# Kernel optimization log

Measured on AMD Instinct MI355X. Metric: run time of the kernel, lower is better.

## Reference

```python
import jax, jax.numpy as jnp
import numpy as np

N, E, G = 16384, 65536, 512
T, FIN, FOUT = 4, 128, 32
_DEG_HIST = np.array([1.0, 2.0, 3.0, 4.0])
AVG_LOG = float((np.log(np.arange(4) + 1.0) * _DEG_HIST).sum() / _DEG_HIST.sum())


def _bn(x, g, b, eps=1e-5):
    # BatchNorm1d in training mode: biased batch stats
    m = x.mean(0)
    v = x.var(0)
    return (x - m) * jax.lax.rsqrt(v + eps) * g + b


def _pna_conv(x, edge_index, ea_raw, We_c, be_c, Wpre, bpre, Wpost, bpost, Wlin, blin):
    src, dst = edge_index[0], edge_index[1]
    ea = ea_raw @ We_c + be_c                                   # conv-internal edge encoder [E,FIN]
    xt = jnp.broadcast_to(x[:, None, :], (N, T, FIN))           # towers share input (divide_input=False)
    h = jnp.concatenate([xt[dst], xt[src],
                         jnp.broadcast_to(ea[:, None, :], (E, T, FIN))], axis=-1)  # [E,T,3*FIN]
    m = jnp.einsum('etf,tfg->etg', h, Wpre) + bpre              # per-tower pre-NN [E,T,FIN]
    deg = jnp.clip(jax.ops.segment_sum(jnp.ones((E,), x.dtype), dst, N), 1.0)
    inv = (1.0 / deg)[:, None, None]
    mean = jax.ops.segment_sum(m, dst, N) * inv
    mean2 = jax.ops.segment_sum(m * m, dst, N) * inv
    std = jnp.sqrt(jax.nn.relu(mean2 - mean * mean) + 1e-5)
    mn = jax.ops.segment_min(m, dst, N)
    mx = jax.ops.segment_max(m, dst, N)
    mn = jnp.where(jnp.isfinite(mn), mn, 0.0)
    mx = jnp.where(jnp.isfinite(mx), mx, 0.0)
    agg = jnp.concatenate([mean, mn, mx, std], axis=-1)         # [N,T,4*FIN]
    s = (jnp.log(deg + 1.0) / AVG_LOG)[:, None, None]           # amplification scaler
    out = jnp.concatenate([agg, agg * s, agg / s], axis=-1)     # identity|amp|attenuation [N,T,12*FIN]
    out = jnp.concatenate([xt, out], axis=-1)                   # [N,T,13*FIN]
    out = jnp.einsum('ntf,tfg->ntg', out, Wpost) + bpost        # per-tower post-NN [N,T,FOUT]
    return out.reshape(N, T * FOUT) @ Wlin + blin               # tower mixing [N,FIN]


def setup_inputs() -> dict:
    key = jax.random.key(0)
    ks = jax.random.split(key, 24)
    def rn(k, shape, scale=0.05):
        return jax.random.normal(k, shape, dtype=jnp.float32) * scale
    return dict(
        x=jax.random.normal(ks[0], (N, 11), jnp.float32),
        edge_attr=jax.random.uniform(ks[1], (E, 4), jnp.float32),
        edge_index=jax.random.randint(ks[2], (2, E), 0, N),
        batch=jnp.sort(jax.random.randint(ks[3], (N,), 0, G)),
        Wa=rn(ks[4], (11, FIN), 0.2), ba=rn(ks[5], (FIN,)),
        We=rn(ks[6], (4, FIN), 0.2), be=rn(ks[7], (FIN,)),
        We_conv=rn(ks[8], (3, FIN, FIN)), be_conv=rn(ks[9], (3, FIN)),
        Wpre=rn(ks[10], (3, T, 3 * FIN, FIN)), bpre=rn(ks[11], (3, T, FIN)),
        Wpost=rn(ks[12], (3, T, 13 * FIN, FOUT)), bpost=rn(ks[13], (3, T, FOUT)),
        Wlin=rn(ks[14], (3, FIN, FIN)), blin=rn(ks[15], (3, FIN)),
        bng=1.0 + rn(ks[16], (3, FIN)), bnb=rn(ks[17], (3, FIN)),
        W1=rn(ks[18], (FIN, 64), 0.1), b1=rn(ks[19], (64,)),
        hg=1.0 + rn(ks[20], (64,)), hb=rn(ks[21], (64,)),
        W2=rn(ks[22], (64, 1), 0.1), b2=rn(ks[23], (1,)),
    )


def reference(x, edge_attr, edge_index, batch, Wa, ba, We, be,
              We_conv, be_conv, Wpre, bpre, Wpost, bpost, Wlin, blin,
              bng, bnb, W1, b1, hg, hb, W2, b2):
    h = jax.nn.relu(x @ Wa + ba)
    ea = jax.nn.relu(edge_attr @ We + be)
    for l in range(3):
        h = jax.nn.relu(_bn(_pna_conv(h, edge_index, ea, We_conv[l], be_conv[l],
                                      Wpre[l], bpre[l], Wpost[l], bpost[l],
                                      Wlin[l], blin[l]), bng[l], bnb[l]))
    cnt = jnp.clip(jax.ops.segment_sum(jnp.ones((N,), h.dtype), batch, G), 1.0)
    pooled = jax.ops.segment_sum(h, batch, G) / cnt[:, None]    # global_mean_pool
    z = jax.nn.relu(pooled @ W1 + b1)
    z = _bn(z, hg, hb)
    return (z @ W2 + b2).reshape(-1)
```

## Files before the change

### kernel.cpp

```cpp
#include <hip/hip_runtime.h>
#include <hip/hip_bf16.h>

#define DEVFN static __device__ __forceinline__

constexpr int NN = 16384;
constexpr int EE = 65536;
constexpr int GG = 512;
constexpr float AVG_LOG_F = 1.0227308671603782f;

typedef _Float16 hfrag __attribute__((ext_vector_type(8)));
typedef __attribute__((ext_vector_type(4))) float f4;

DEVFN unsigned short f2h(float f) {
  _Float16 h = (_Float16)f;
  unsigned short r; __builtin_memcpy(&r, &h, 2); return r;
}
DEVFN float h2f(unsigned short s) {
  _Float16 h; __builtin_memcpy(&h, &s, 2); return (float)h;
}

DEVFN float4 ld4hf(const unsigned short* p) {
  ushort4 u = *(const ushort4*)p;
  float4 r;
  r.x = h2f(u.x); r.y = h2f(u.y); r.z = h2f(u.z); r.w = h2f(u.w);
  return r;
}

DEVFN int swk(int row, int k) {
  return (k & ~31) + ((((k >> 3) & 3) ^ ((row >> 1) & 3)) << 3) + (k & 7);
}

DEVFN void gll16(const unsigned short* g, unsigned short* l) {
  __builtin_amdgcn_global_load_lds(
      (__attribute__((address_space(1))) void*)g,
      (__attribute__((address_space(3))) void*)l, 16, 0, 0);
}

struct AuxP {
  const float* p0;
  const float* p1;
  const float* p2;
  const float* p3;
  const float* p4;
};

template <int ASRC, int NT, bool BIAS, bool RELU, bool OHALF>
__global__ __launch_bounds__(256) void mgemm(
    const void* __restrict__ Av, const unsigned short* __restrict__ WT,
    const float* __restrict__ bias,
    float* __restrict__ C, AuxP aux,
    int Nc, int K, int lda, int ldc,
    long long bsA, long long bsW, long long bsC, int bsBias)
{
  constexpr bool COPYA = (ASRC == 1);
  constexpr int BST = NT * 16 * 32;

  const int z = blockIdx.z;
  WT += (long long)z * bsW;
  if (BIAS) bias += (long long)z * bsBias;
  float* Cf = C + (OHALF ? 0 : (long long)z * bsC);
  unsigned short* Cu = (unsigned short*)C + (OHALF ? (long long)z * bsC : 0);

  __shared__ __align__(16) unsigned short AhS[2 * 128 * 32];
  __shared__ __align__(16) unsigned short BhS[2 * BST];

  const int tid = threadIdx.x;
  const long long bm = (long long)blockIdx.x * 128;
  const int bn = blockIdx.y * (NT * 16);
  const int w = tid >> 6;
  const int lane = tid & 63;
  const int quad = lane >> 4;
  const int c16 = lane & 15;
  const int srow = lane >> 2;
  const int sslot = (lane & 3) << 3;

  const int arow = tid >> 1;
  const int sel = tid & 1;
  const long long rowsrc = bm + arow;

  f4 acc[2][NT];
#pragma unroll
  for (int mt = 0; mt < 2; ++mt)
#pragma unroll
    for (int nt = 0; nt < NT; ++nt) acc[mt][nt] = (f4){0.f, 0.f, 0.f, 0.f};

  const unsigned short* whp = WT + (long long)(bn + srow) * K + sslot;

  const unsigned short* ahp = nullptr;
  if (COPYA)
    ahp = (const unsigned short*)Av + (long long)z * bsA + (bm + srow) * (long long)lda + sslot;

  float invdc = 1.f;
  float sv = 0.f, iv = 0.f;
  const float* apA = nullptr;
  const float* Prow_base = nullptr;
  const float* pxp_base = nullptr;
  if (!COPYA) {
    if (ASRC == 3) {
      Prow_base = aux.p0 + rowsrc * 384;
      pxp_base = aux.p1 + rowsrc * 128;
      sv = aux.p2[rowsrc];
      iv = aux.p3[rowsrc];
    } else {
      apA = (const float*)Av + (long long)z * bsA + rowsrc * lda;
      invdc = 1.f / fmaxf(aux.p0[rowsrc], 1.f);
    }
  }
  const int swa = (arow >> 1) & 3;
  const int s0us = arow * 32 + (((2 * sel) ^ swa) << 3);
  const int s1us = arow * 32 + (((2 * sel + 1) ^ swa) << 3);

  const int swr8 = ((quad ^ ((c16 >> 1) & 3)) << 3);

  auto stageB = [&](int bi, int k0) {
#pragma unroll
    for (int ch = w; ch < NT; ch += 4)
      gll16(whp + (long long)ch * 16 * K + k0, BhS + bi * BST + ch * 512);
  };
  auto stageA = [&](int bi, int k0) {
#pragma unroll
    for (int ch = w; ch < 8; ch += 4)
      gll16(ahp + (long long)ch * 16 * lda + k0, AhS + bi * 4096 + ch * 512);
  };
  auto stageLoad = [&](int k0, float* va) {
    const int ck0 = k0 + sel * 16;
    if (ASRC == 3) {
      const float* Prow = Prow_base + ((ck0 >> 5) * 96) + (ck0 & 31);
      const float* pxp = pxp_base + ck0;
#pragma unroll
      for (int i = 0; i < 16; ++i)
        va[i] = pxp[i] + Prow[i] + sv * Prow[32 + i] + iv * Prow[64 + i] +
                aux.p4[ck0 + i];
    } else {
      *(float4*)&va[0] = *(const float4*)(apA + ck0);
      *(float4*)&va[4] = *(const float4*)(apA + ck0 + 4);
      *(float4*)&va[8] = *(const float4*)(apA + ck0 + 8);
      *(float4*)&va[12] = *(const float4*)(apA + ck0 + 12);
    }
  };
  auto stageWrite = [&](int bi, const float* va) {
    hfrag hv0, hv1;
#pragma unroll
    for (int i = 0; i < 16; ++i) {
      float x = va[i];
      if (ASRC == 4) x *= invdc;
      if (i < 8) hv0[i] = (_Float16)x;
      else       hv1[i - 8] = (_Float16)x;
    }
    *(hfrag*)&AhS[bi * 4096 + s0us] = hv0;
    *(hfrag*)&AhS[bi * 4096 + s1us] = hv1;
  };
  auto fragmfma = [&](int bi) {
    hfrag ah[2];
#pragma unroll
    for (int mt = 0; mt < 2; ++mt) {
      const int r = w * 32 + mt * 16 + c16;
      ah[mt] = *(const hfrag*)&AhS[bi * 4096 + r * 32 + swr8];
    }
#pragma unroll
    for (int nt = 0; nt < NT; ++nt) {
      const int r = nt * 16 + c16;
      hfrag bh = *(const hfrag*)&BhS[bi * BST + r * 32 + swr8];
#pragma unroll
      for (int mt = 0; mt < 2; ++mt)
        acc[mt][nt] = __builtin_amdgcn_mfma_f32_16x16x32_f16(ah[mt], bh, acc[mt][nt], 0, 0, 0);
    }
  };

  float va[16];
  const int nk = K >> 5;

  if (COPYA) {
    stageA(0, 0);
    stageB(0, 0);
  } else {
    stageLoad(0, va);
    stageB(0, 0);
    stageWrite(0, va);
  }
  __syncthreads();

  for (int kt = 0; kt < nk; ++kt) {
    const int bi = kt & 1;
    const bool pf = (kt + 1 < nk);
    if (pf) {
      stageB(bi ^ 1, (kt + 1) << 5);
      if (COPYA) stageA(bi ^ 1, (kt + 1) << 5);
      else stageLoad((kt + 1) << 5, va);
    }
    fragmfma(bi);
    if (!COPYA && pf) stageWrite(bi ^ 1, va);
    __syncthreads();
  }

#pragma unroll
  for (int nt = 0; nt < NT; ++nt) {
    int col = bn + nt * 16 + c16;
    if (col >= Nc) continue;
    float bv = BIAS ? bias[col] : 0.f;
#pragma unroll
    for (int mt = 0; mt < 2; ++mt) {
#pragma unroll
      for (int r = 0; r < 4; ++r) {
        long long row = bm + w * 32 + mt * 16 + quad * 4 + r;
        float v = acc[mt][nt][r] + bv;
        if (RELU) v = fmaxf(v, 0.f);
        if (OHALF) Cu[row * ldc + col] = f2h(v);
        else Cf[row * ldc + col] = v;
      }
    }
  }
}

__global__ void node_enc(const float* __restrict__ x, const float* __restrict__ Wa,
                         const float* __restrict__ ba, unsigned short* __restrict__ hb)
{
  int n = blockIdx.x, c = threadIdx.x;
  float acc = ba[c];
#pragma unroll
  for (int k = 0; k < 11; ++k) acc += x[n * 11 + k] * Wa[k * 128 + c];
  hb[((long long)n << 7) + swk(n, c)] = f2h(fmaxf(acc, 0.f));
}

__global__ void edge_enc(const float* __restrict__ eat, const float* __restrict__ We,
                         const float* __restrict__ be, const int* __restrict__ slot_of,
                         unsigned short* __restrict__ ef)
{
  int e = blockIdx.x, c = threadIdx.x;
  float acc = be[c];
#pragma unroll
  for (int k = 0; k < 4; ++k) acc += eat[e * 4 + k] * We[k * 128 + c];
  long long slot = slot_of[e];
  ef[slot * 128 + swk((int)slot, c)] = f2h(fmaxf(acc, 0.f));
}

__global__ void count_deg(const int* __restrict__ dst, int* __restrict__ degi)
{
  int e = blockIdx.x * 256 + threadIdx.x;
  if (e < EE) atomicAdd(&degi[dst[e]], 1);
}

__global__ __launch_bounds__(1024) void scan_k(const int* __restrict__ degi,
                                               int* __restrict__ row_off,
                                               int* __restrict__ cursor,
                                               float* __restrict__ s_arr,
                                               float* __restrict__ invs)
{
  __shared__ int tsum[1024];
  int t = threadIdx.x;
  int local[16];
  int base = t * 16;
  int s = 0;
#pragma unroll
  for (int i = 0; i < 16; ++i) { local[i] = s; s += degi[base + i]; }
  tsum[t] = s;
  __syncthreads();
  for (int off = 1; off < 1024; off <<= 1) {
    int v = (t >= off) ? tsum[t - off] : 0;
    __syncthreads();
    tsum[t] += v;
    __syncthreads();
  }
  int prev = (t == 0) ? 0 : tsum[t - 1];
#pragma unroll
  for (int i = 0; i < 16; ++i) {
    int start = prev + local[i];
    row_off[base + i] = start;
    cursor[base + i] = start;
    int cnt = degi[base + i];
    float degc = fmaxf((float)cnt, 1.f);
    float sv = logf(degc + 1.f) / AVG_LOG_F;
    s_arr[base + i] = sv;
    invs[base + i] = 1.f / sv;
  }
  if (t == 1023) row_off[NN] = tsum[1023];
}

__global__ void scatter_k(const int* __restrict__ src, const int* __restrict__ dst,
                          int* __restrict__ cursor,
                          int* __restrict__ slot_of, int* __restrict__ esrc)
{
  int e = blockIdx.x * 256 + threadIdx.x;
  if (e >= EE) return;
  int d = dst[e];
  int slot = atomicAdd(&cursor[d], 1);
  slot_of[e] = slot;
  esrc[slot] = src[e];
}

__global__ __launch_bounds__(512) void fold_w(const float* __restrict__ We_conv,
                                              const float* __restrict__ Wpre,
                                              float* __restrict__ Wfold)
{
  int k = blockIdx.x & 127, l = blockIdx.x >> 7;
  int t = threadIdx.x >> 7, f = threadIdx.x & 127;
  const float* wc = We_conv + (long long)(l * 128 + k) * 128;
  const float* wp = Wpre + ((long long)((l * 4 + t) * 384 + 256)) * 128 + f;
  float acc = 0.f;
  for (int j = 0; j < 128; ++j) acc += wc[j] * wp[(long long)j * 128];
  Wfold[((long long)(l * 128 + k)) * 512 + threadIdx.x] = acc;
}

__global__ __launch_bounds__(512) void fold_b(const float* __restrict__ be_conv,
                                              const float* __restrict__ Wpre,
                                              const float* __restrict__ bpre,
                                              float* __restrict__ bfold)
{
  int l = blockIdx.x;
  int t = threadIdx.x >> 7, f = threadIdx.x & 127;
  const float* bc = be_conv + l * 128;
  const float* wp = Wpre + ((long long)((l * 4 + t) * 384 + 256)) * 128 + f;
  float acc = bpre[(l * 4 + t) * 128 + f];
  for (int j = 0; j < 128; ++j) acc += bc[j] * wp[(long long)j * 128];
  bfold[l * 512 + threadIdx.x] = acc;
}

__global__ void tsplit_preAB(const float* __restrict__ Wpre,
                             unsigned short* __restrict__ o)
{
  int b = blockIdx.x;
  int lt = b >> 8, n = b & 255, k = threadIdx.x;
  int row = (n < 128) ? k : (128 + k);
  int f = n & 127;
  float v = Wpre[((long long)(lt * 384 + row)) * 128 + f];
  o[((long long)(lt * 256 + n)) * 128 + swk(n, k)] = f2h(v);
}

__global__ void tsplit_fold(const float* __restrict__ Wfold,
                            unsigned short* __restrict__ o)
{
  int b = blockIdx.x;
  int lt = b >> 7, n = b & 127, k = threadIdx.x;
  int l = lt >> 2, t = lt & 3;
  float v = Wfold[((long long)(l * 128 + k)) * 512 + t * 128 + n];
  o[((long long)(lt * 128 + n)) * 128 + swk(n, k)] = f2h(v);
}

__global__ __launch_bounds__(512) void tsplit_post3(const float* __restrict__ Wpost,
                                                    unsigned short* __restrict__ o)
{
  int b = blockIdx.x;
  int lt = b >> 7, c = b & 127;
  int r = threadIdx.x;
  float v = 0.f;
  if (c < 96)
    v = Wpost[((long long)(lt * 1664 + 128 + (c >> 5) * 512 + r)) * 32 + (c & 31)];
  o[((long long)(lt * 128 + c)) * 512 + swk(c, r)] = f2h(v);
}

__global__ void tsplit_wx(const float* __restrict__ Wpost,
                          unsigned short* __restrict__ o)
{
  int b = blockIdx.x;
  int l = b >> 7, c = b & 127, k = threadIdx.x;
  float v = Wpost[((long long)((l * 4 + (c >> 5)) * 1664 + k)) * 32 + (c & 31)];
  o[((long long)(l * 128 + c)) * 128 + swk(c, k)] = f2h(v);
}

__global__ void tsplit_lin(const float* __restrict__ Wlin,
                           unsigned short* __restrict__ o)
{
  int b = blockIdx.x;
  int l = b >> 7, n = b & 127, k = threadIdx.x;
  float v = Wlin[((long long)(l * 128 + k)) * 128 + n];
  o[((long long)(l * 128 + n)) * 128 + swk(n, k)] = f2h(v);
}

__global__ void tsplit_w1(const float* __restrict__ W1,
                          unsigned short* __restrict__ o)
{
  int n = blockIdx.x;
  int k = threadIdx.x;
  o[(long long)n * 128 + swk(n, k)] = f2h(W1[k * 64 + n]);
}

__global__ __launch_bounds__(256) void aggregate_ct(
    const unsigned short* __restrict__ ABb, const unsigned short* __restrict__ Mb,
    const int* __restrict__ row_off, const int* __restrict__ esrc,
    unsigned short* __restrict__ aggs)
{
  const int tid = threadIdx.x;
  const int c4 = (tid & 31) << 2;
  const int z = (tid >> 5) & 3;
  const int n = blockIdx.x * 2 + (tid >> 7);
  const unsigned short* M = Mb + (long long)z * EE * 128;
  const unsigned short* ABs = ABb + (long long)z * NN * 256;
  unsigned short* ag = aggs + (long long)z * NN * 512;
  const int beg = row_off[n], end = row_off[n + 1];
  const int cnt = end - beg;
  const float degc = fmaxf((float)cnt, 1.0f);
  const float4 aval = ld4hf(&ABs[(long long)n * 256 + c4]);

  float sum[4] = {0.f, 0.f, 0.f, 0.f}, sq[4] = {0.f, 0.f, 0.f, 0.f};
  float mn[4] = {INFINITY, INFINITY, INFINITY, INFINITY};
  float mx[4] = {-INFINITY, -INFINITY, -INFINITY, -INFINITY};

  auto upd = [&](const float4& mv, const float4& bv) {
    float m0 = aval.x + bv.x + mv.x;
    float m1 = aval.y + bv.y + mv.y;
    float m2 = aval.z + bv.z + mv.z;
    float m3 = aval.w + bv.w + mv.w;
    sum[0] += m0; sq[0] += m0 * m0; mn[0] = fminf(mn[0], m0); mx[0] = fmaxf(mx[0], m0);
    sum[1] += m1; sq[1] += m1 * m1; mn[1] = fminf(mn[1], m1); mx[1] = fmaxf(mx[1], m1);
    sum[2] += m2; sq[2] += m2 * m2; mn[2] = fminf(mn[2], m2); mx[2] = fmaxf(mx[2], m2);
    sum[3] += m3; sq[3] += m3 * m3; mn[3] = fminf(mn[3], m3); mx[3] = fmaxf(mx[3], m3);
  };

  for (int s0 = beg; s0 < end; s0 += 4) {
    const int e1 = min(s0 + 1, end - 1);
    const int e2 = min(s0 + 2, end - 1);
    const int e3 = min(s0 + 3, end - 1);
    const int sA = esrc[s0], sB = esrc[e1], sC = esrc[e2], sD = esrc[e3];
    const float4 mA = ld4hf(&M[(long long)s0 * 128 + c4]);
    const float4 mB = ld4hf(&M[(long long)e1 * 128 + c4]);
    const float4 mC = ld4hf(&M[(long long)e2 * 128 + c4]);
    const float4 mD = ld4hf(&M[(long long)e3 * 128 + c4]);
    const float4 bA = ld4hf(&ABs[(long long)sA * 256 + 128 + c4]);
    const float4 bB = ld4hf(&ABs[(long long)sB * 256 + 128 + c4]);
    const float4 bC = ld4hf(&ABs[(long long)sC * 256 + 128 + c4]);
    const float4 bD = ld4hf(&ABs[(long long)sD * 256 + 128 + c4]);
    upd(mA, bA);
    if (s0 + 1 < end) upd(mB, bB);
    if (s0 + 2 < end) upd(mC, bC);
    if (s0 + 3 < end) upd(mD, bD);
  }

  const float inv = 1.0f / degc;
  float mean[4], stdv[4];
#pragma unroll
  for (int j = 0; j < 4; ++j) {
    mean[j] = sum[j] * inv;
    float var = sq[j] * inv - mean[j] * mean[j];
    stdv[j] = sqrtf(fmaxf(var, 0.f) + 1e-5f);
    if (cnt == 0) { mn[j] = 0.f; mx[j] = 0.f; }
  }
  const int sc = swk(n, c4);
  const long long base = (long long)n * 512 + sc;
  ushort4 o;
  o.x = f2h(mean[0]); o.y = f2h(mean[1]); o.z = f2h(mean[2]); o.w = f2h(mean[3]);
  *(ushort4*)&ag[base] = o;
  o.x = f2h(mn[0]); o.y = f2h(mn[1]); o.z = f2h(mn[2]); o.w = f2h(mn[3]);
  *(ushort4*)&ag[base + 128] = o;
  o.x = f2h(mx[0]); o.y = f2h(mx[1]); o.z = f2h(mx[2]); o.w = f2h(mx[3]);
  *(ushort4*)&ag[base + 256] = o;
  o.x = f2h(stdv[0]); o.y = f2h(stdv[1]); o.z = f2h(stdv[2]); o.w = f2h(stdv[3]);
  *(ushort4*)&ag[base + 384] = o;
}

__global__ __launch_bounds__(256) void bn_partial(const float* __restrict__ y,
                                                  float* __restrict__ colsum,
                                                  float* __restrict__ colsq)
{
  int c = threadIdx.x & 127;
  int rh = threadIdx.x >> 7;
  int r0 = blockIdx.x * 128;
  float s = 0.f, q = 0.f;
  for (int r = r0 + rh; r < r0 + 128; r += 2) {
    float v = y[(long long)r * 128 + c];
    s += v;
    q += v * v;
  }
  __shared__ float ps[256], pq[256];
  ps[threadIdx.x] = s;
  pq[threadIdx.x] = q;
  __syncthreads();
  if (threadIdx.x < 128) {
    atomicAdd(&colsum[c], ps[c] + ps[c + 128]);
    atomicAdd(&colsq[c], pq[c] + pq[c + 128]);
  }
}

__global__ void bn_coef(const float* __restrict__ colsum, const float* __restrict__ colsq,
                        const float* __restrict__ g, const float* __restrict__ b,
                        float* __restrict__ coef)
{
  int c = threadIdx.x;
  float mean = colsum[c] * (1.f / 16384.f);
  float var = colsq[c] * (1.f / 16384.f) - mean * mean;
  float sc = g[c] * rsqrtf(var + 1e-5f);
  coef[c] = sc;
  coef[128 + c] = b[c] - mean * sc;
}

__global__ __launch_bounds__(256) void bn_apply(const float* __restrict__ y,
                                                const float* __restrict__ coef,
                                                unsigned short* __restrict__ hb)
{
  int idx = blockIdx.x * 256 + threadIdx.x;
  int c = idx & 127, n = idx >> 7;
  float v = fmaxf(y[idx] * coef[c] + coef[128 + c], 0.f);
  hb[((long long)n << 7) + swk(n, c)] = f2h(v);
}

__global__ void pool_add(const float* __restrict__ y, const float* __restrict__ colsum,
                         const float* __restrict__ colsq, const float* __restrict__ g,
                         const float* __restrict__ b, const int* __restrict__ batch,
                         float* __restrict__ pooled, float* __restrict__ cntf)
{
  int n = blockIdx.x, c = threadIdx.x;
  float mean = colsum[c] * (1.f / 16384.f);
  float var = colsq[c] * (1.f / 16384.f) - mean * mean;
  float v = fmaxf((y[(long long)n * 128 + c] - mean) * rsqrtf(var + 1e-5f) * g[c] + b[c], 0.f);
  int bb = batch[n];
  atomicAdd(&pooled[(long long)bb * 128 + c], v);
  if (c == 0) atomicAdd(&cntf[bb], 1.f);
}

__global__ __launch_bounds__(256) void zstats(const float* __restrict__ z,
                                              float* __restrict__ zm, float* __restrict__ zv)
{
  int j = blockIdx.x;
  float s = 0.f, q = 0.f;
  for (int g = threadIdx.x; g < GG; g += 256) {
    float v = z[g * 64 + j];
    s += v;
    q += v * v;
  }
  __shared__ float ps[256], pq[256];
  ps[threadIdx.x] = s;
  pq[threadIdx.x] = q;
  __syncthreads();
  for (int st = 128; st > 0; st >>= 1) {
    if (threadIdx.x < st) {
      ps[threadIdx.x] += ps[threadIdx.x + st];
      pq[threadIdx.x] += pq[threadIdx.x + st];
    }
    __syncthreads();
  }
  if (threadIdx.x == 0) {
    float m = ps[0] / (float)GG;
    zm[j] = m;
    zv[j] = pq[0] / (float)GG - m * m;
  }
}

__global__ void final_out(const float* __restrict__ z, const float* __restrict__ zm,
                          const float* __restrict__ zv, const float* __restrict__ hg,
                          const float* __restrict__ hb, const float* __restrict__ W2,
                          const float* __restrict__ b2, float* __restrict__ out)
{
  int g = blockIdx.x;
  int j = threadIdx.x;
  float v = (z[g * 64 + j] - zm[j]) * rsqrtf(zv[j] + 1e-5f) * hg[j] + hb[j];
  float t = v * W2[j];
#pragma unroll
  for (int off = 32; off > 0; off >>= 1) t += __shfl_down(t, off);
  if (j == 0) out[g] = t + b2[0];
}

extern "C" void kernel_launch(void* const* d_in, const int* in_sizes, int n_in,
                              void* d_out, int out_size, void* d_ws, size_t ws_size,
                              hipStream_t stream)
{
  (void)in_sizes; (void)n_in; (void)out_size;
  const float* x = (const float*)d_in[0];
  const float* eat = (const float*)d_in[1];
  const int* ei = (const int*)d_in[2];
  const int* batch = (const int*)d_in[3];
  const float* Wa = (const float*)d_in[4];
  const float* ba = (const float*)d_in[5];
  const float* We = (const float*)d_in[6];
  const float* be = (const float*)d_in[7];
  const float* We_conv = (const float*)d_in[8];
  const float* be_conv = (const float*)d_in[9];
  const float* Wpre = (const float*)d_in[10];
  const float* bpre = (const float*)d_in[11];
  const float* Wpost = (const float*)d_in[12];
  const float* bpost = (const float*)d_in[13];
  const float* Wlin = (const float*)d_in[14];
  const float* blin = (const float*)d_in[15];
  const float* bng = (const float*)d_in[16];
  const float* bnb = (const float*)d_in[17];
  const float* W1 = (const float*)d_in[18];
  const float* b1 = (const float*)d_in[19];
  const float* hg = (const float*)d_in[20];
  const float* hb = (const float*)d_in[21];
  const float* W2 = (const float*)d_in[22];
  const float* b2 = (const float*)d_in[23];
  float* out = (float*)d_out;

  const int* srcI = ei;
  const int* dstI = ei + EE;

  char* ws = (char*)d_ws;
  size_t off = 0;
  auto alloc = [&](size_t bytes) -> char* {
    char* p = ws + off;
    off += (bytes + 255) & ~(size_t)255;
    return p;
  };

  unsigned short* hbf = (unsigned short*)alloc((size_t)NN * 128 * 2);
  float* hn = (float*)alloc((size_t)NN * 128 * 4);
  unsigned short* eaf = (unsigned short*)alloc((size_t)EE * 128 * 2);
  unsigned short* AB = (unsigned short*)alloc((size_t)4 * NN * 256 * 2);
  char* Mregion = alloc((size_t)4 * EE * 128 * 2);
  unsigned short* Mb = (unsigned short*)Mregion;
  float* P = (float*)Mregion;
  float* Px = (float*)(Mregion + (size_t)NN * 384 * 4);
  unsigned short* aggt = (unsigned short*)alloc((size_t)4 * NN * 512 * 2);
  float* s_arr = (float*)alloc((size_t)NN * 4);
  float* invs = (float*)alloc((size_t)NN * 4);
  int* degi = (int*)alloc((size_t)NN * 4);
  int* cursor = (int*)alloc((size_t)NN * 4);
  int* row_off = (int*)alloc((size_t)(NN + 1) * 4);
  int* slot_of = (int*)alloc((size_t)EE * 4);
  int* esrc = (int*)alloc((size_t)EE * 4);
  float* WfoldF = (float*)alloc((size_t)3 * 128 * 512 * 4);
  float* bfold = (float*)alloc((size_t)3 * 512 * 4);
  unsigned short* preABT = (unsigned short*)alloc((size_t)12 * 256 * 128 * 2);
  unsigned short* foldT = (unsigned short*)alloc((size_t)12 * 128 * 128 * 2);
  unsigned short* post3T = (unsigned short*)alloc((size_t)12 * 128 * 512 * 2);
  unsigned short* wxT = (unsigned short*)alloc((size_t)3 * 128 * 128 * 2);
  unsigned short* linT = (unsigned short*)alloc((size_t)3 * 128 * 128 * 2);
  unsigned short* w1T = (unsigned short*)alloc((size_t)64 * 128 * 2);
  float* colstats = (float*)alloc(512 * 4);
  float* bncoef = (float*)alloc(256 * 4);
  float* pooled = (float*)alloc((size_t)GG * 128 * 4);
  float* cntf = (float*)alloc((size_t)GG * 4);
  float* zbuf = (float*)alloc((size_t)GG * 64 * 4);
  float* zm = (float*)alloc(64 * 4);
  float* zv = (float*)alloc(64 * 4);

  if (off > ws_size) return;

  float* cs[2] = {colstats, colstats + 256};

  hipMemsetAsync(degi, 0, (size_t)NN * 4, stream);
  count_deg<<<EE / 256, 256, 0, stream>>>(dstI, degi);
  scan_k<<<1, 1024, 0, stream>>>(degi, row_off, cursor, s_arr, invs);
  scatter_k<<<EE / 256, 256, 0, stream>>>(srcI, dstI, cursor, slot_of, esrc);

  node_enc<<<NN, 128, 0, stream>>>(x, Wa, ba, hbf);
  edge_enc<<<EE, 128, 0, stream>>>(eat, We, be, slot_of, eaf);
  fold_w<<<384, 512, 0, stream>>>(We_conv, Wpre, WfoldF);
  fold_b<<<3, 512, 0, stream>>>(be_conv, Wpre, bpre, bfold);
  tsplit_preAB<<<12 * 256, 128, 0, stream>>>(Wpre, preABT);
  tsplit_fold<<<12 * 128, 128, 0, stream>>>(WfoldF, foldT);
  tsplit_post3<<<12 * 128, 512, 0, stream>>>(Wpost, post3T);
  tsplit_wx<<<3 * 128, 128, 0, stream>>>(Wpost, wxT);
  tsplit_lin<<<3 * 128, 128, 0, stream>>>(Wlin, linT);
  tsplit_w1<<<64, 128, 0, stream>>>(W1, w1T);

  for (int l = 0; l < 3; ++l) {
    hipMemsetAsync(cs[l & 1], 0, 256 * 4, stream);
    mgemm<1, 8, false, false, true><<<dim3(NN / 128, 2, 4), 256, 0, stream>>>(
        hbf, preABT + (size_t)l * 4 * 256 * 128, nullptr, (float*)AB, AuxP{},
        256, 128, 128, 256, 0, (long long)256 * 128, (long long)NN * 256, 0);
    mgemm<1, 8, true, false, true><<<dim3(EE / 128, 1, 4), 256, 0, stream>>>(
        eaf, foldT + (size_t)l * 4 * 128 * 128, bfold + l * 512, (float*)Mb, AuxP{},
        128, 128, 128, 128, 0, (long long)128 * 128, (long long)EE * 128, 128);
    aggregate_ct<<<dim3(NN / 2, 1, 1), 256, 0, stream>>>(AB, Mb, row_off, esrc, aggt);
    mgemm<1, 6, false, false, false><<<dim3(NN / 128, 1, 4), 256, 0, stream>>>(
        aggt, post3T + (size_t)l * 4 * 128 * 512, nullptr, P, AuxP{},
        96, 512, 512, 384, (long long)NN * 512, (long long)128 * 512, 96, 0);
    mgemm<1, 8, false, false, false><<<dim3(NN / 128, 1, 1), 256, 0, stream>>>(
        hbf, wxT + (size_t)l * 128 * 128, nullptr, Px, AuxP{},
        128, 128, 128, 128, 0, 0, 0, 0);
    mgemm<3, 8, true, false, false><<<dim3(NN / 128, 1, 1), 256, 0, stream>>>(
        nullptr, linT + (size_t)l * 128 * 128, blin + l * 128, hn,
        AuxP{P, Px, s_arr, invs, bpost + l * 128},
        128, 128, 128, 128, 0, 0, 0, 0);
    bn_partial<<<128, 256, 0, stream>>>(hn, cs[l & 1], cs[l & 1] + 128);
    if (l < 2) {
      bn_coef<<<1, 128, 0, stream>>>(cs[l & 1], cs[l & 1] + 128,
                                     bng + l * 128, bnb + l * 128, bncoef);
      bn_apply<<<NN * 128 / 256, 256, 0, stream>>>(hn, bncoef, hbf);
    }
  }

  hipMemsetAsync(pooled, 0, (size_t)GG * 128 * 4, stream);
  hipMemsetAsync(cntf, 0, (size_t)GG * 4, stream);
  pool_add<<<NN, 128, 0, stream>>>(hn, cs[0], cs[0] + 128,
                                   bng + 2 * 128, bnb + 2 * 128, batch, pooled, cntf);
  mgemm<4, 4, true, true, false><<<dim3(GG / 128, 1, 1), 256, 0, stream>>>(
      pooled, w1T, b1, zbuf, AuxP{cntf, nullptr, nullptr, nullptr, nullptr},
      64, 128, 128, 64, 0, 0, 0, 0);
  zstats<<<64, 256, 0, stream>>>(zbuf, zm, zv);
  final_out<<<GG, 64, 0, stream>>>(zbuf, zm, zv, hg, hb, W2, b2, out);
}
```

Measured before the change: 656.2 us.

## Fold Wx@Wlin into lin GEMM, fuse BN stats, merge weight packing kernels

Precomputes the product of the post-NN x-branch weights and Wlin, then extends the final lin GEMM to K=256. Its first half takes the P-derived activations and its second half streams hbf directly, which removes the separate Px GEMM and its fp32 round trip. The lin GEMM epilogue now accumulates BatchNorm column sums and squares through shared and global atomics, replacing the bn_partial pass over hn. The six weight-transpose kernels are merged into one pack_all launch. The cost is a different fp16 rounding order from pre-multiplying the weights, plus extra atomics in the epilogue.

```diff
diff --git a/kernel.cpp b/kernel.cpp
--- a/kernel.cpp
+++ b/kernel.cpp
@@ -87,24 +87,20 @@
   const unsigned short* whp = WT + (long long)(bn + srow) * K + sslot;
 
   const unsigned short* ahp = nullptr;
-  if (COPYA)
+  if (COPYA || ASRC == 3)
     ahp = (const unsigned short*)Av + (long long)z * bsA + (bm + srow) * (long long)lda + sslot;
 
   float invdc = 1.f;
   float sv = 0.f, iv = 0.f;
   const float* apA = nullptr;
   const float* Prow_base = nullptr;
-  const float* pxp_base = nullptr;
-  if (!COPYA) {
-    if (ASRC == 3) {
-      Prow_base = aux.p0 + rowsrc * 384;
-      pxp_base = aux.p1 + rowsrc * 128;
-      sv = aux.p2[rowsrc];
-      iv = aux.p3[rowsrc];
-    } else {
-      apA = (const float*)Av + (long long)z * bsA + rowsrc * lda;
-      invdc = 1.f / fmaxf(aux.p0[rowsrc], 1.f);
-    }
+  if (ASRC == 3) {
+    Prow_base = aux.p0 + rowsrc * 384;
+    sv = aux.p2[rowsrc];
+    iv = aux.p3[rowsrc];
+  } else if (ASRC == 4) {
+    apA = (const float*)Av + (long long)z * bsA + rowsrc * lda;
+    invdc = 1.f / fmaxf(aux.p0[rowsrc], 1.f);
   }
   const int swa = (arow >> 1) & 3;
   const int s0us = arow * 32 + (((2 * sel) ^ swa) << 3);
@@ -126,11 +122,9 @@
     const int ck0 = k0 + sel * 16;
     if (ASRC == 3) {
       const float* Prow = Prow_base + ((ck0 >> 5) * 96) + (ck0 & 31);
-      const float* pxp = pxp_base + ck0;
 #pragma unroll
       for (int i = 0; i < 16; ++i)
-        va[i] = pxp[i] + Prow[i] + sv * Prow[32 + i] + iv * Prow[64 + i] +
-                aux.p4[ck0 + i];
+        va[i] = Prow[i] + sv * Prow[32 + i] + iv * Prow[64 + i] + aux.p4[ck0 + i];
     } else {
       *(float4*)&va[0] = *(const float4*)(apA + ck0);
       *(float4*)&va[4] = *(const float4*)(apA + ck0 + 4);
@@ -183,16 +177,27 @@
   for (int kt = 0; kt < nk; ++kt) {
     const int bi = kt & 1;
     const bool pf = (kt + 1 < nk);
+    bool nextds = false;
     if (pf) {
-      stageB(bi ^ 1, (kt + 1) << 5);
-      if (COPYA) stageA(bi ^ 1, (kt + 1) << 5);
-      else stageLoad((kt + 1) << 5, va);
+      const int k0 = (kt + 1) << 5;
+      stageB(bi ^ 1, k0);
+      if (COPYA) {
+        stageA(bi ^ 1, k0);
+      } else if (ASRC == 3 && k0 >= 128) {
+        stageA(bi ^ 1, k0 - 128);
+      } else {
+        stageLoad(k0, va);
+        nextds = true;
+      }
     }
     fragmfma(bi);
-    if (!COPYA && pf) stageWrite(bi ^ 1, va);
+    if (nextds) stageWrite(bi ^ 1, va);
     __syncthreads();
   }
 
+  float ls[NT], lq[NT];
+#pragma unroll
+  for (int nt = 0; nt < NT; ++nt) { ls[nt] = 0.f; lq[nt] = 0.f; }
 #pragma unroll
   for (int nt = 0; nt < NT; ++nt) {
     int col = bn + nt * 16 + c16;
@@ -205,9 +210,29 @@
         long long row = bm + w * 32 + mt * 16 + quad * 4 + r;
         float v = acc[mt][nt][r] + bv;
         if (RELU) v = fmaxf(v, 0.f);
+        if (ASRC == 3) { ls[nt] += v; lq[nt] += v * v; }
         if (OHALF) Cu[row * ldc + col] = f2h(v);
         else Cf[row * ldc + col] = v;
       }
+    }
+  }
+  if constexpr (ASRC == 3) {
+    float* csum = (float*)AhS;
+    float* csq = csum + 128;
+    if (tid < 256 && tid >= 128) {}
+    if (tid < 128) { csum[tid] = 0.f; csq[tid] = 0.f; }
+    __syncthreads();
+#pragma unroll
+    for (int nt = 0; nt < NT; ++nt) {
+      int col = bn + nt * 16 + c16;
+      atomicAdd(&csum[col], ls[nt]);
+      atomicAdd(&csq[col], lq[nt]);
+    }
+    __syncthreads();
+    float* colsum = (float*)aux.p1;
+    if (tid < 128) {
+      atomicAdd(&colsum[tid], csum[tid]);
+      atomicAdd(&colsum[128 + tid], csq[tid]);
     }
   }
 }
@@ -315,63 +340,57 @@
   bfold[l * 512 + threadIdx.x] = acc;
 }
 
-__global__ void tsplit_preAB(const float* __restrict__ Wpre,
-                             unsigned short* __restrict__ o)
-{
-  int b = blockIdx.x;
-  int lt = b >> 8, n = b & 255, k = threadIdx.x;
-  int row = (n < 128) ? k : (128 + k);
-  int f = n & 127;
-  float v = Wpre[((long long)(lt * 384 + row)) * 128 + f];
-  o[((long long)(lt * 256 + n)) * 128 + swk(n, k)] = f2h(v);
-}
-
-__global__ void tsplit_fold(const float* __restrict__ Wfold,
-                            unsigned short* __restrict__ o)
-{
-  int b = blockIdx.x;
-  int lt = b >> 7, n = b & 127, k = threadIdx.x;
-  int l = lt >> 2, t = lt & 3;
-  float v = Wfold[((long long)(l * 128 + k)) * 512 + t * 128 + n];
-  o[((long long)(lt * 128 + n)) * 128 + swk(n, k)] = f2h(v);
-}
-
-__global__ __launch_bounds__(512) void tsplit_post3(const float* __restrict__ Wpost,
-                                                    unsigned short* __restrict__ o)
-{
-  int b = blockIdx.x;
-  int lt = b >> 7, c = b & 127;
-  int r = threadIdx.x;
-  float v = 0.f;
-  if (c < 96)
-    v = Wpost[((long long)(lt * 1664 + 128 + (c >> 5) * 512 + r)) * 32 + (c & 31)];
-  o[((long long)(lt * 128 + c)) * 512 + swk(c, r)] = f2h(v);
-}
-
-__global__ void tsplit_wx(const float* __restrict__ Wpost,
-                          unsigned short* __restrict__ o)
-{
-  int b = blockIdx.x;
-  int l = b >> 7, c = b & 127, k = threadIdx.x;
-  float v = Wpost[((long long)((l * 4 + (c >> 5)) * 1664 + k)) * 32 + (c & 31)];
-  o[((long long)(l * 128 + c)) * 128 + swk(c, k)] = f2h(v);
-}
-
-__global__ void tsplit_lin(const float* __restrict__ Wlin,
-                           unsigned short* __restrict__ o)
-{
-  int b = blockIdx.x;
-  int l = b >> 7, n = b & 127, k = threadIdx.x;
-  float v = Wlin[((long long)(l * 128 + k)) * 128 + n];
-  o[((long long)(l * 128 + n)) * 128 + swk(n, k)] = f2h(v);
-}
-
-__global__ void tsplit_w1(const float* __restrict__ W1,
-                          unsigned short* __restrict__ o)
-{
-  int n = blockIdx.x;
-  int k = threadIdx.x;
-  o[(long long)n * 128 + swk(n, k)] = f2h(W1[k * 64 + n]);
+__global__ __launch_bounds__(128) void pack_all(
+    const float* __restrict__ Wpre, const float* __restrict__ WfoldF,
+    const float* __restrict__ Wpost, const float* __restrict__ Wlin,
+    const float* __restrict__ W1,
+    unsigned short* __restrict__ preABT, unsigned short* __restrict__ foldT,
+    unsigned short* __restrict__ post3T, unsigned short* __restrict__ linT2,
+    unsigned short* __restrict__ w1T)
+{
+  const int b = blockIdx.x;
+  const int t = threadIdx.x;
+  if (b < 3072) {
+    int lt = b >> 8, n = b & 255, k = t;
+    int row = (n < 128) ? k : (128 + k);
+    int f = n & 127;
+    float v = Wpre[((long long)(lt * 384 + row)) * 128 + f];
+    preABT[((long long)(lt * 256 + n)) * 128 + swk(n, k)] = f2h(v);
+  } else if (b < 4608) {
+    int b2 = b - 3072;
+    int lt = b2 >> 7, n = b2 & 127, k = t;
+    int l = lt >> 2, tw = lt & 3;
+    float v = WfoldF[((long long)(l * 128 + k)) * 512 + tw * 128 + n];
+    foldT[((long long)(lt * 128 + n)) * 128 + swk(n, k)] = f2h(v);
+  } else if (b < 6144) {
+    int b3 = b - 4608;
+    int lt = b3 >> 7, c = b3 & 127;
+#pragma unroll
+    for (int j = 0; j < 4; ++j) {
+      int r = t + 128 * j;
+      float v = 0.f;
+      if (c < 96)
+        v = Wpost[((long long)(lt * 1664 + 128 + (c >> 5) * 512 + r)) * 32 + (c & 31)];
+      post3T[((long long)(lt * 128 + c)) * 512 + swk(c, r)] = f2h(v);
+    }
+  } else if (b < 6528) {
+    int b4 = b - 6144;
+    int l = b4 >> 7, n = b4 & 127, k = t;
+    float v = Wlin[((long long)(l * 128 + k)) * 128 + n];
+    linT2[((long long)(l * 128 + n)) * 256 + swk(n, k)] = f2h(v);
+  } else if (b < 6912) {
+    int b5 = b - 6528;
+    int l = b5 >> 7, kk = b5 & 127, o = t;
+    float acc = 0.f;
+    for (int c = 0; c < 128; ++c) {
+      float wx = Wpost[((long long)((l * 4 + (c >> 5)) * 1664 + kk)) * 32 + (c & 31)];
+      acc += wx * Wlin[((long long)(l * 128 + c)) * 128 + o];
+    }
+    linT2[((long long)(l * 128 + o)) * 256 + swk(o, 128 + kk)] = f2h(acc);
+  } else {
+    int n = b - 6912, k = t;
+    w1T[(long long)n * 128 + swk(n, k)] = f2h(W1[k * 64 + n]);
+  }
 }
 
 __global__ __launch_bounds__(256) void aggregate_ct(
@@ -445,29 +464,6 @@
   *(ushort4*)&ag[base + 256] = o;
   o.x = f2h(stdv[0]); o.y = f2h(stdv[1]); o.z = f2h(stdv[2]); o.w = f2h(stdv[3]);
   *(ushort4*)&ag[base + 384] = o;
-}
-
-__global__ __launch_bounds__(256) void bn_partial(const float* __restrict__ y,
-                                                  float* __restrict__ colsum,
-                                                  float* __restrict__ colsq)
-{
-  int c = threadIdx.x & 127;
-  int rh = threadIdx.x >> 7;
-  int r0 = blockIdx.x * 128;
-  float s = 0.f, q = 0.f;
-  for (int r = r0 + rh; r < r0 + 128; r += 2) {
-    float v = y[(long long)r * 128 + c];
-    s += v;
-    q += v * v;
-  }
-  __shared__ float ps[256], pq[256];
-  ps[threadIdx.x] = s;
-  pq[threadIdx.x] = q;
-  __syncthreads();
-  if (threadIdx.x < 128) {
-    atomicAdd(&colsum[c], ps[c] + ps[c + 128]);
-    atomicAdd(&colsq[c], pq[c] + pq[c + 128]);
-  }
 }
 
 __global__ void bn_coef(const float* __restrict__ colsum, const float* __restrict__ colsq,
@@ -597,7 +593,6 @@
   char* Mregion = alloc((size_t)4 * EE * 128 * 2);
   unsigned short* Mb = (unsigned short*)Mregion;
   float* P = (float*)Mregion;
-  float* Px = (float*)(Mregion + (size_t)NN * 384 * 4);
   unsigned short* aggt = (unsigned short*)alloc((size_t)4 * NN * 512 * 2);
   float* s_arr = (float*)alloc((size_t)NN * 4);
   float* invs = (float*)alloc((size_t)NN * 4);
@@ -611,8 +606,7 @@
   unsigned short* preABT = (unsigned short*)alloc((size_t)12 * 256 * 128 * 2);
   unsigned short* foldT = (unsigned short*)alloc((size_t)12 * 128 * 128 * 2);
   unsigned short* post3T = (unsigned short*)alloc((size_t)12 * 128 * 512 * 2);
-  unsigned short* wxT = (unsigned short*)alloc((size_t)3 * 128 * 128 * 2);
-  unsigned short* linT = (unsigned short*)alloc((size_t)3 * 128 * 128 * 2);
+  unsigned short* linT2 = (unsigned short*)alloc((size_t)3 * 128 * 256 * 2);
   unsigned short* w1T = (unsigned short*)alloc((size_t)64 * 128 * 2);
   float* colstats = (float*)alloc(512 * 4);
   float* bncoef = (float*)alloc(256 * 4);
@@ -635,12 +629,8 @@
   edge_enc<<<EE, 128, 0, stream>>>(eat, We, be, slot_of, eaf);
   fold_w<<<384, 512, 0, stream>>>(We_conv, Wpre, WfoldF);
   fold_b<<<3, 512, 0, stream>>>(be_conv, Wpre, bpre, bfold);
-  tsplit_preAB<<<12 * 256, 128, 0, stream>>>(Wpre, preABT);
-  tsplit_fold<<<12 * 128, 128, 0, stream>>>(WfoldF, foldT);
-  tsplit_post3<<<12 * 128, 512, 0, stream>>>(Wpost, post3T);
-  tsplit_wx<<<3 * 128, 128, 0, stream>>>(Wpost, wxT);
-  tsplit_lin<<<3 * 128, 128, 0, stream>>>(Wlin, linT);
-  tsplit_w1<<<64, 128, 0, stream>>>(W1, w1T);
+  pack_all<<<6976, 128, 0, stream>>>(Wpre, WfoldF, Wpost, Wlin, W1,
+                                     preABT, foldT, post3T, linT2, w1T);
 
   for (int l = 0; l < 3; ++l) {
     hipMemsetAsync(cs[l & 1], 0, 256 * 4, stream);
@@ -654,14 +644,10 @@
     mgemm<1, 6, false, false, false><<<dim3(NN / 128, 1, 4), 256, 0, stream>>>(
         aggt, post3T + (size_t)l * 4 * 128 * 512, nullptr, P, AuxP{},
         96, 512, 512, 384, (long long)NN * 512, (long long)128 * 512, 96, 0);
-    mgemm<1, 8, false, false, false><<<dim3(NN / 128, 1, 1), 256, 0, stream>>>(
-        hbf, wxT + (size_t)l * 128 * 128, nullptr, Px, AuxP{},
-        128, 128, 128, 128, 0, 0, 0, 0);
     mgemm<3, 8, true, false, false><<<dim3(NN / 128, 1, 1), 256, 0, stream>>>(
-        nullptr, linT + (size_t)l * 128 * 128, blin + l * 128, hn,
-        AuxP{P, Px, s_arr, invs, bpost + l * 128},
-        128, 128, 128, 128, 0, 0, 0, 0);
-    bn_partial<<<128, 256, 0, stream>>>(hn, cs[l & 1], cs[l & 1] + 128);
+        hbf, linT2 + (size_t)l * 128 * 256, blin + l * 128, hn,
+        AuxP{P, cs[l & 1], s_arr, invs, bpost + l * 128},
+        128, 256, 128, 128, 0, 0, 0, 0);
     if (l < 2) {
       bn_coef<<<1, 128, 0, stream>>>(cs[l & 1], cs[l & 1] + 128,
                                      bng + l * 128, bnb + l * 128, bncoef);
```

Result: faster. 596.7 us (-9.1%).
